# Kernel optimization log

Hardware: AMD Instinct MI355X
Metric: run time of the kernel (lower is better)

Reference implementation:

```python
import jax, jax.numpy as jnp
import numpy as np

N, D, HID, G, E2 = 2048, 256, 128, 8, 16384


def _mlp(h, w1, b1, g, be, w2, b2):
    # Linear -> ReLU -> BatchNorm1d (training mode, biased batch var) -> Linear
    h = jax.nn.relu(h @ w1 + b1)
    mu = h.mean(axis=0)
    var = ((h - mu) ** 2).mean(axis=0)
    h = (h - mu) / jnp.sqrt(var + 1e-5) * g + be
    return h @ w2 + b2


def setup_inputs() -> dict:
    key = jax.random.key(0)
    ks = jax.random.split(key, 12)
    x = jax.random.normal(ks[0], (N, D), jnp.float32)
    src = jax.random.randint(ks[1], (E2,), 0, N)
    dst = jax.random.randint(ks[2], (E2,), 0, N)
    src = jnp.where(src == dst, (src + 1) % N, src)  # no self loops
    edge_index = jnp.stack([jnp.concatenate([src, dst]),
                            jnp.concatenate([dst, src])])  # symmetric
    batch = jnp.sort(jax.random.randint(ks[3], (N,), 0, G))
    def lin(k, i, o):
        return 0.1 * jax.random.normal(k, (i, o), jnp.float32)
    out = dict(x=x, edge_index=edge_index, batch=batch)
    dims = [(1, HID, HID), (HID, HID, HID), (HID, HID, 1)]
    names = [("w11", "b11", "g1", "be1", "w12", "b12"),
             ("w21", "b21", "g2", "be2", "w22", "b22"),
             ("w31", "b31", "g3", "be3", "w32", "b32")]
    k = 4
    for (i, h, o), n in zip(dims, names):
        out[n[0]] = lin(ks[k], i, h)
        out[n[1]] = jnp.zeros((h,), jnp.float32)
        out[n[2]] = jnp.ones((h,), jnp.float32)
        out[n[3]] = jnp.zeros((h,), jnp.float32)
        out[n[4]] = lin(ks[k + 1], h, o)
        out[n[5]] = jnp.zeros((o,), jnp.float32)
        k += 2
    return out


def reference(x, edge_index, batch,
              w11, b11, g1, be1, w12, b12,
              w21, b21, g2, be2, w22, b22,
              w31, b31, g3, be3, w32, b32):
    n = x.shape[0]
    # dense adjacency from edge_index; L = D - A (unnormalized graph Laplacian)
    A = jnp.zeros((n, n), x.dtype).at[edge_index[0], edge_index[1]].set(1.0)
    deg = A.sum(axis=1)
    # entropy term: V = x*(Lx) - x*(Ax) + A(x*x), Lx = deg*x - Ax
    Ax = A @ x
    V = x * (deg[:, None] * x - Ax) - x * Ax + A @ (x * x)
    V = jnp.linalg.norm(V, axis=1)  # [n]
    # per-graph softmax over the batch segments
    mx = jax.ops.segment_max(V, batch, num_segments=G)
    ex = jnp.exp(V - mx[batch])
    P = ex / jax.ops.segment_sum(ex, batch, num_segments=G)[batch]
    P = jnp.where(P == 0.0, 1.0, P)
    ent = -P * jnp.log(P)  # [n]

    # GINConv (eps=0): mlp(x + sum_{j in N(i)} x_j) = mlp(x + A @ x)
    def gin(h, w1, b1, g, be, w2, b2):
        return _mlp(h + A @ h, w1, b1, g, be, w2, b2)

    h = gin(ent[:, None], w11, b11, g1, be1, w12, b12)
    h = gin(h, w21, b21, g2, be2, w22, b22)
    h = gin(h, w31, b31, g3, be3, w32, b32)
    p = jax.nn.sigmoid(h[:, 0])  # [n] node probabilities

    gamma = ent.sum()
    loss = gamma - jnp.vdot(ent, p) + jnp.vdot(p, A @ p)

    # greedy conditional expectation (sequential MIS-style selection)
    order = jnp.argsort(-p)

    def step(carry, idx):
        dummy, sel, rej = carry
        nb = A[idx] > 0.0  # neighbor mask [n]
        deg0 = ~jnp.any(nb)
        sel = sel.at[idx].set(sel[idx] | deg0)  # isolated node -> selected
        eligible = (~rej[idx]) & (~sel[idx])
        s = jnp.where(nb, 0.0, dummy).at[idx].set(1.0)
        li = gamma - jnp.vdot(ent, s) + jnp.vdot(s, A @ s)
        accept = eligible & (li <= loss)
        sel = sel.at[idx].set(sel[idx] | accept)
        rej = rej | (nb & accept)
        dummy = jnp.where(accept, s, dummy)
        return (dummy, sel, rej), None

    init = (p, jnp.zeros(n, dtype=bool), jnp.zeros(n, dtype=bool))
    (dummy, sel, rej), _ = jax.lax.scan(step, init, order)

    # graph reconstruction (masked instead of compacted, for static shapes)
    mask = sel.astype(x.dtype)
    x_pooled = x * mask[:, None]
    A2 = A @ A
    A3 = A2 @ A
    eye = jnp.eye(n, dtype=x.dtype)
    adj_pooled = (1.0 - eye) * jnp.clip(A2 + A3, 0.0, 1.0) * (mask[:, None] * mask[None, :])
    batch_pooled = jnp.where(sel, batch, -1)
    return x_pooled, adj_pooled, sel, batch_pooled, loss
```

## Files before the change

### kernel.cpp

```cpp
#include <hip/hip_runtime.h>
#include <math.h>

#define NN 2048
#define DIMF 256
#define HIDN 128
#define NG 8
#define NEDGES 32768
#define W32 32
#define TRI_CAP 131072
#define TRI_LDS 4864

typedef unsigned long long u64;
typedef unsigned char u8;
typedef unsigned short u16;

__global__ void k_init(u64* __restrict__ rowbits, int* __restrict__ segstart) {
  int i = blockIdx.x * blockDim.x + threadIdx.x;
  for (int k = i; k < NN * W32; k += gridDim.x * blockDim.x) rowbits[k] = 0ull;
  if (i <= NG) segstart[i] = NN;
}

__global__ void k_edges(const int* __restrict__ ei, u64* __restrict__ rowbits) {
  int e = blockIdx.x * blockDim.x + threadIdx.x;
  if (e >= NEDGES) return;
  int u = ei[e], v = ei[NEDGES + e];
  atomicOr(&rowbits[((size_t)u << 5) + (v >> 6)], 1ull << (v & 63));
}

__global__ void k_deg(const u64* __restrict__ rowbits, int* __restrict__ deg,
                      const int* __restrict__ batch, int* __restrict__ segstart) {
  int i = blockIdx.x * blockDim.x + threadIdx.x;
  if (i >= NN) return;
  int c = 0;
  for (int w = 0; w < W32; ++w) c += __popcll(rowbits[(i << 5) + w]);
  deg[i] = c;
  if (i == 0 || batch[i] != batch[i - 1]) segstart[batch[i]] = i;
}

__global__ void k_scan2048(const int* __restrict__ in, int* __restrict__ out) {
  __shared__ int part[256];
  int t = threadIdx.x;
  int v[8]; int s = 0;
  for (int k = 0; k < 8; ++k) { v[k] = in[t * 8 + k]; s += v[k]; }
  part[t] = s;
  __syncthreads();
  for (int off = 1; off < 256; off <<= 1) {
    int y = (t >= off) ? part[t - off] : 0;
    __syncthreads();
    part[t] += y;
    __syncthreads();
  }
  int run = part[t] - s;
  for (int k = 0; k < 8; ++k) { out[t * 8 + k] = run; run += v[k]; }
  if (t == 255) out[NN] = part[255];
}

__global__ void k_extract(const u64* __restrict__ rowbits, const int* __restrict__ rp,
                          int* __restrict__ col, int* __restrict__ cnt) {
  int i = blockIdx.x * blockDim.x + threadIdx.x;
  if (i >= NN) return;
  const u64* ri = rowbits + ((size_t)i << 5);
  int o = rp[i];
  for (int w = 0; w < W32; ++w) {
    u64 b = ri[w];
    while (b) { col[o++] = (w << 6) + __builtin_ctzll(b); b &= b - 1; }
  }
  int c = 0;
  for (int e = rp[i]; e < o; ++e) {
    const u64* ra = rowbits + ((size_t)col[e] << 5);
    for (int w = 0; w < W32; ++w) c += __popcll(ra[w] & ri[w]);
  }
  cnt[i] = c;
}

__global__ void k_trifill(const u64* __restrict__ rowbits, const int* __restrict__ rp,
                          const int* __restrict__ col, const int* __restrict__ tp,
                          int2* __restrict__ tri) {
  int i = blockIdx.x * blockDim.x + threadIdx.x;
  if (i >= NN) return;
  const u64* ri = rowbits + ((size_t)i << 5);
  int o = tp[i];
  for (int e = rp[i]; e < rp[i + 1]; ++e) {
    int a = col[e];
    const u64* ra = rowbits + ((size_t)a << 5);
    for (int w = 0; w < W32; ++w) {
      u64 b = ra[w] & ri[w];
      while (b) {
        int j = (w << 6) + __builtin_ctzll(b);
        if (o < TRI_CAP) tri[o] = make_int2(a, j);
        ++o;
        b &= b - 1;
      }
    }
  }
}

__global__ void k_V(const float* __restrict__ x, const int* __restrict__ rp,
                    const int* __restrict__ col, float* __restrict__ V) {
  int i = blockIdx.x; int t = threadIdx.x;
  float xi = x[i * DIMF + t];
  float s1 = 0.f, s2 = 0.f;
  int r0 = rp[i], r1 = rp[i + 1];
  for (int e = r0; e < r1; ++e) {
    float xj = x[col[e] * DIMF + t];
    s1 += xj; s2 += xj * xj;
  }
  float dg = (float)(r1 - r0);
  float val = dg * xi * xi - 2.f * xi * s1 + s2;
  __shared__ double red[DIMF];
  red[t] = (double)val * (double)val;
  __syncthreads();
  for (int off = DIMF / 2; off > 0; off >>= 1) { if (t < off) red[t] += red[t + off]; __syncthreads(); }
  if (t == 0) V[i] = (float)sqrt(red[0]);
}

__global__ void k_soft(const float* __restrict__ V, const int* __restrict__ segstart,
                       float* __restrict__ ent, double* __restrict__ seggamma) {
  int g = blockIdx.x; int t = threadIdx.x;
  int s = segstart[g];
  int e = NN;
  for (int gg = g + 1; gg <= NG; ++gg) { int v = segstart[gg]; if (v < e) e = v; }
  if (s >= e) { if (t == 0) seggamma[g] = 0.0; return; }
  __shared__ float fm[256];
  __shared__ double dd[256];
  float m = -3.0e38f;
  for (int i = s + t; i < e; i += 256) m = fmaxf(m, V[i]);
  fm[t] = m; __syncthreads();
  for (int off = 128; off > 0; off >>= 1) { if (t < off) fm[t] = fmaxf(fm[t], fm[t + off]); __syncthreads(); }
  float mx = fm[0];
  __syncthreads();
  double sum = 0.0;
  for (int i = s + t; i < e; i += 256) sum += exp((double)V[i] - (double)mx);
  dd[t] = sum; __syncthreads();
  for (int off = 128; off > 0; off >>= 1) { if (t < off) dd[t] += dd[t + off]; __syncthreads(); }
  double tot = dd[0];
  __syncthreads();
  double gs = 0.0;
  for (int i = s + t; i < e; i += 256) {
    double P = exp((double)V[i] - (double)mx) / tot;
    float ev = (P > 0.0) ? (float)(-P * log(P)) : 0.f;
    ent[i] = ev;
    gs += (double)ev;
  }
  dd[t] = gs; __syncthreads();
  for (int off = 128; off > 0; off >>= 1) { if (t < off) dd[t] += dd[t + off]; __syncthreads(); }
  if (t == 0) seggamma[g] = dd[0];
}

__global__ void k_agg1(const float* __restrict__ ent, const int* __restrict__ rp,
                       const int* __restrict__ col, float* __restrict__ agg) {
  int i = blockIdx.x * blockDim.x + threadIdx.x;
  if (i >= NN) return;
  float a = ent[i];
  for (int e = rp[i]; e < rp[i + 1]; ++e) a += ent[col[e]];
  agg[i] = a;
}

__global__ void k_lin1(const float* __restrict__ agg, const float* __restrict__ w,
                       const float* __restrict__ b, float* __restrict__ t) {
  int idx = blockIdx.x * blockDim.x + threadIdx.x;
  if (idx >= NN * HIDN) return;
  int i = idx >> 7, k = idx & 127;
  float v = agg[i] * w[k] + b[k];
  t[idx] = v > 0.f ? v : 0.f;
}

__global__ void k_bn(const float* __restrict__ t, const float* __restrict__ g,
                     const float* __restrict__ be, float* __restrict__ scale,
                     float* __restrict__ shift) {
  int k = blockIdx.x; int tid = threadIdx.x;
  __shared__ double red[256];
  double s = 0.0;
  for (int i = tid; i < NN; i += 256) s += (double)t[i * HIDN + k];
  red[tid] = s; __syncthreads();
  for (int off = 128; off > 0; off >>= 1) { if (tid < off) red[tid] += red[tid + off]; __syncthreads(); }
  double mu = red[0] / NN;
  __syncthreads();
  double v = 0.0;
  for (int i = tid; i < NN; i += 256) { double dv = (double)t[i * HIDN + k] - mu; v += dv * dv; }
  red[tid] = v; __syncthreads();
  for (int off = 128; off > 0; off >>= 1) { if (tid < off) red[tid] += red[tid + off]; __syncthreads(); }
  if (tid == 0) {
    float var = (float)(red[0] / NN);
    float sc = g[k] / sqrtf(var + 1e-5f);
    scale[k] = sc;
    shift[k] = be[k] - (float)mu * sc;
  }
}

template<int PRE, int RELU>
__global__ void k_mm(const float* __restrict__ in, const float* __restrict__ Wm,
                     const float* __restrict__ bias, const float* __restrict__ scale,
                     const float* __restrict__ shift, float* __restrict__ out) {
  __shared__ float ti[8][HIDN];
  int r0 = blockIdx.x * 8; int t = threadIdx.x;
  for (int r = 0; r < 8; ++r) {
    float v = in[(r0 + r) * HIDN + t];
    if (PRE) v = v * scale[t] + shift[t];
    ti[r][t] = v;
  }
  __syncthreads();
  float acc[8];
  #pragma unroll
  for (int r = 0; r < 8; ++r) acc[r] = 0.f;
  for (int k = 0; k < HIDN; ++k) {
    float w = Wm[k * HIDN + t];
    #pragma unroll
    for (int r = 0; r < 8; ++r) acc[r] += ti[r][k] * w;
  }
  for (int r = 0; r < 8; ++r) {
    float v = acc[r] + bias[t];
    if (RELU) v = fmaxf(v, 0.f);
    out[(r0 + r) * HIDN + t] = v;
  }
}

__global__ void k_agg128(const float* __restrict__ h, const int* __restrict__ rp,
                         const int* __restrict__ col, float* __restrict__ agg) {
  int i = blockIdx.x; int t = threadIdx.x;
  float a = h[i * HIDN + t];
  for (int e = rp[i]; e < rp[i + 1]; ++e) a += h[col[e] * HIDN + t];
  agg[i * HIDN + t] = a;
}

__global__ void k_lin3(const float* __restrict__ tn, const float* __restrict__ scale,
                       const float* __restrict__ shift, const float* __restrict__ w32,
                       const float* __restrict__ b32, float* __restrict__ p) {
  int i = blockIdx.x; int t = threadIdx.x;
  float v = (tn[i * HIDN + t] * scale[t] + shift[t]) * w32[t];
  __shared__ float red[HIDN];
  red[t] = v; __syncthreads();
  for (int off = 64; off > 0; off >>= 1) { if (t < off) red[t] += red[t + off]; __syncthreads(); }
  if (t == 0) {
    float h3 = red[0] + b32[0];
    p[i] = 1.f / (1.f + expf(-h3));
  }
}

__global__ void k_q0(const float* __restrict__ p, const float* __restrict__ ent,
                     const int* __restrict__ rp, const int* __restrict__ col,
                     float* __restrict__ q0, float* __restrict__ e0) {
  int i = blockIdx.x * blockDim.x + threadIdx.x;
  if (i >= NN) return;
  float s = 0.f, es = 0.f;
  for (int e = rp[i]; e < rp[i + 1]; ++e) {
    int j = col[e];
    float pj = p[j];
    s += pj; es += ent[j] * pj;
  }
  q0[i] = s; e0[i] = es;
}

__global__ void k_loss(const float* __restrict__ ent, const float* __restrict__ p,
                       const float* __restrict__ q0, const double* __restrict__ seggamma,
                       double* __restrict__ scal) {
  __shared__ double ra[256], rb[256];
  int t = threadIdx.x;
  double a = 0.0, b = 0.0;
  for (int i = t; i < NN; i += 256) { a += (double)ent[i] * (double)p[i]; b += (double)p[i] * (double)q0[i]; }
  ra[t] = a; rb[t] = b; __syncthreads();
  for (int off = 128; off > 0; off >>= 1) {
    if (t < off) { ra[t] += ra[t + off]; rb[t] += rb[t + off]; }
    __syncthreads();
  }
  if (t == 0) {
    double gamma = 0.0;
    for (int g = 0; g < NG; ++g) gamma += seggamma[g];
    scal[0] = gamma; scal[1] = ra[0]; scal[2] = rb[0];
    scal[3] = gamma - ra[0] + rb[0];
  }
}

__global__ void k_sort(const float* __restrict__ p, int* __restrict__ order) {
  __shared__ u64 s[NN];
  int t = threadIdx.x;
  for (int k = t; k < NN; k += 1024) {
    unsigned b = __float_as_uint(p[k]);
    unsigned ss = (b & 0x80000000u) ? ~b : (b | 0x80000000u);
    s[k] = ((u64)(~ss) << 32) | (unsigned)k;
  }
  __syncthreads();
  for (int k = 2; k <= NN; k <<= 1) {
    for (int j = k >> 1; j > 0; j >>= 1) {
      for (int i = t; i < NN; i += 1024) {
        int ixj = i ^ j;
        if (ixj > i) {
          bool up = ((i & k) == 0);
          u64 a = s[i], b = s[ixj];
          if ((a > b) == up) { s[i] = b; s[ixj] = a; }
        }
      }
      __syncthreads();
    }
  }
  order[t] = (int)(s[t] & 0xFFFFFFFFull);
  order[t + 1024] = (int)(s[t + 1024] & 0xFFFFFFFFull);
}

#define DPP2(ctrl)                                                                        \
  a += __int_as_float(__builtin_amdgcn_update_dpp(0, __float_as_int(a), ctrl, 0xf, 0xf, true)); \
  b += __int_as_float(__builtin_amdgcn_update_dpp(0, __float_as_int(b), ctrl, 0xf, 0xf, true));

__device__ __forceinline__ void red2(float& a, float& b) {
  DPP2(0x111)
  DPP2(0x112)
  DPP2(0x114)
  DPP2(0x118)
  DPP2(0x142)
  DPP2(0x143)
  a = __int_as_float(__builtin_amdgcn_readlane(__float_as_int(a), 63));
  b = __int_as_float(__builtin_amdgcn_readlane(__float_as_int(b), 63));
}

__global__ void __launch_bounds__(1024, 1) k_greedy(
    const int* __restrict__ rp, const int* __restrict__ col,
    const int* __restrict__ tp, const int2* __restrict__ tri,
    const int* __restrict__ order, const float* __restrict__ p,
    const float* __restrict__ ent, const float* __restrict__ q0,
    const float* __restrict__ e0, const double* __restrict__ scal,
    u8* __restrict__ selb_g) {
  __shared__ float2 dq[NN];
  __shared__ float2 ee[NN];
  __shared__ u16 colL[NEDGES];
  __shared__ u16 ordl[NN];
  __shared__ uint2 rtP[NN + 1];
  __shared__ ushort2 triL[TRI_LDS];
  __shared__ unsigned decidedL[64], selL[64];
  __shared__ unsigned maskL[2];
  __shared__ float4 svA[2][16];
  int t = threadIdx.x;
  int w = t >> 6, lane = t & 63;

  for (int i = t; i < NN; i += 1024) {
    dq[i] = make_float2(p[i], q0[i]);
    ee[i] = make_float2(ent[i], e0[i]);
    ordl[i] = (u16)order[i];
    int tv0 = tp[i]; if (tv0 > 65535) tv0 = 65535;
    int tv1 = tp[i + 1]; if (tv1 > 65535) tv1 = 65535;
    rtP[i] = make_uint2((unsigned)rp[i] | ((unsigned)tv0 << 16),
                        (unsigned)rp[i + 1] | ((unsigned)tv1 << 16));
  }
  for (int i = t; i < NEDGES; i += 1024) colL[i] = (u16)col[i];
  for (int i = t; i < TRI_LDS; i += 1024) {
    int2 ab = tri[i];
    triL[i] = make_ushort2((u16)(ab.x & 2047), (u16)(ab.y & 2047));
  }
  if (t < 64) { decidedL[t] = 0u; selL[t] = 0u; }
  if (t < 2) maskL[t] = 0u;
  double gamma = scal[0], loss = scal[3];
  double ed = scal[1], dAd = scal[2];
  __syncthreads();
  for (int i = t; i < NN; i += 1024) {
    if (((rtP[i].y & 0xffffu) - (rtP[i].x & 0xffffu)) == 0u) {
      atomicOr(&decidedL[i >> 5], 1u << (i & 31));
      atomicOr(&selL[i >> 5], 1u << (i & 31));
    }
  }
  __syncthreads();

  int pos = 0, rc = 0;
  while (pos < NN) {
    int b = rc & 1; ++rc;
    int step = pos + w;
    if (step < NN) {
      int idx = ordl[step];
      if (!((decidedL[idx >> 5] >> (idx & 31)) & 1u)) {
        uint2 rt = rtP[idx];
        int r0 = rt.x & 0xffff, r1 = rt.y & 0xffff;
        int t0 = rt.x >> 16, t1 = rt.y >> 16;
        float2 dqi = dq[idx];
        float2 eei = ee[idx];
        float s2 = 0.f, st = 0.f;
        for (int e = r0 + lane; e < r1; e += 64) {
          float2 v = dq[colL[e]];
          s2 -= v.y * v.x;
        }
        if (t1 <= TRI_LDS) {
          for (int e = t0 + lane; e < t1; e += 64) {
            ushort2 ab = triL[e];
            st += dq[ab.x].x * dq[ab.y].x;
          }
        } else {
          int g0 = tp[idx], g1 = tp[idx + 1];
          if (g0 > TRI_CAP) g0 = TRI_CAP;
          if (g1 > TRI_CAP) g1 = TRI_CAP;
          for (int e = g0 + lane; e < g1; e += 64) {
            int2 ab = tri[e];
            st += dq[ab.x].x * dq[ab.y].x;
          }
        }
        red2(s2, st);
        float d0 = 1.f - dqi.x;
        float S1 = -eei.y + eei.x * d0;
        float S2 = s2 + dqi.y * d0;
        float sn = -dqi.y;
        double cross = 2.0 * (double)d0 * (double)sn + (double)st;
        double li = gamma - (ed + (double)S1) + (dAd + 2.0 * (double)S2 + cross);
        if (li <= loss && lane == 0) {
          svA[b][w] = make_float4(S1, S2, d0, st);
          atomicOr(&maskL[b], 1u << w);
        }
      }
    }
    __syncthreads();
    unsigned mask = maskL[b];
    if (mask == 0u) { pos += 16; continue; }
    int k = __builtin_ctz(mask);
    int idx = ordl[pos + k];
    float4 A = svA[b][k];
    float2 dqi = dq[idx];
    uint2 rt = rtP[idx];
    int r0 = rt.x & 0xffff, r1 = rt.y & 0xffff;
    {
      double cross = 2.0 * (double)A.z * (double)(-dqi.y) + (double)A.w;
      ed += (double)A.x;
      dAd += 2.0 * (double)A.y + cross;
    }
    __syncthreads();
    if (t == 0) maskL[b] = 0u;
    for (int e = r0 + w; e < r1; e += 16) {
      int a = colL[e];
      float da = -dq[a].x;
      if (da != 0.f) {
        float ea = ee[a].x;
        uint2 art = rtP[a];
        int b0 = art.x & 0xffff, b1 = art.y & 0xffff;
        for (int eb = b0 + lane; eb < b1; eb += 64) {
          int bb = colL[eb];
          atomicAdd(&dq[bb].y, da);
          atomicAdd(&ee[bb].y, ea * da);
        }
      }
    }
    {
      float ei = ee[idx].x;
      for (int e = r0 + t; e < r1; e += 1024) {
        int bb = colL[e];
        atomicAdd(&dq[bb].y, A.z);
        atomicAdd(&ee[bb].y, ei * A.z);
      }
    }
    __syncthreads();
    if (t == 0) {
      dq[idx].x = 1.f;
      atomicOr(&decidedL[idx >> 5], 1u << (idx & 31));
      atomicOr(&selL[idx >> 5], 1u << (idx & 31));
    }
    for (int e = r0 + t; e < r1; e += 1024) {
      int j = colL[e];
      dq[j].x = 0.f;
      atomicOr(&decidedL[j >> 5], 1u << (j & 31));
    }
    __syncthreads();
    pos += k + 1;
  }
  for (int i = t; i < NN; i += 1024)
    selb_g[i] = (u8)((selL[i >> 5] >> (i & 31)) & 1u);
}

__global__ void k_reach(const u64* __restrict__ src, const int* __restrict__ rp,
                        const int* __restrict__ col, u64* __restrict__ dst) {
  int node = blockIdx.x * 2 + (threadIdx.x >> 5);
  int w = threadIdx.x & 31;
  u64 acc = 0;
  for (int e = rp[node]; e < rp[node + 1]; ++e) acc |= src[((size_t)col[e] << 5) + w];
  dst[((size_t)node << 5) + w] = acc;
}

__global__ void k_out(const u64* __restrict__ row2, const u64* __restrict__ row3,
                      const u8* __restrict__ selb, const float* __restrict__ x,
                      const int* __restrict__ batch, const double* __restrict__ scal,
                      float* __restrict__ o_x, float* __restrict__ o_adj,
                      float* __restrict__ o_sel, float* __restrict__ o_bat,
                      float* __restrict__ o_loss) {
  int idx = blockIdx.x * blockDim.x + threadIdx.x;
  {
    int i = idx >> 11, j = idx & 2047;
    int wo = (i << 5) + (j >> 6);
    u64 b = (row2[wo] | row3[wo]) >> (j & 63);
    o_adj[idx] = ((b & 1ull) && i != j && selb[i] && selb[j]) ? 1.f : 0.f;
  }
  if (idx < NN * DIMF) {
    int i = idx >> 8;
    o_x[idx] = selb[i] ? x[idx] : 0.f;
  }
  if (idx < NN) {
    o_sel[idx] = selb[idx] ? 1.f : 0.f;
    o_bat[idx] = selb[idx] ? (float)batch[idx] : -1.f;
  }
  if (idx == 0) o_loss[0] = (float)scal[3];
}

extern "C" void kernel_launch(void* const* d_in, const int* in_sizes, int n_in,
                              void* d_out, int out_size, void* d_ws, size_t ws_size,
                              hipStream_t stream) {
  const float* x    = (const float*)d_in[0];
  const int*   ei   = (const int*)d_in[1];
  const int*   batch= (const int*)d_in[2];
  const float* w11  = (const float*)d_in[3];
  const float* b11  = (const float*)d_in[4];
  const float* g1   = (const float*)d_in[5];
  const float* be1  = (const float*)d_in[6];
  const float* w12  = (const float*)d_in[7];
  const float* b12  = (const float*)d_in[8];
  const float* w21  = (const float*)d_in[9];
  const float* b21  = (const float*)d_in[10];
  const float* g2   = (const float*)d_in[11];
  const float* be2  = (const float*)d_in[12];
  const float* w22  = (const float*)d_in[13];
  const float* b22  = (const float*)d_in[14];
  const float* w31  = (const float*)d_in[15];
  const float* b31  = (const float*)d_in[16];
  const float* g3   = (const float*)d_in[17];
  const float* be3  = (const float*)d_in[18];
  const float* w32  = (const float*)d_in[19];
  const float* b32  = (const float*)d_in[20];

  char* wsb = (char*)d_ws;
  size_t cur = 0;
  auto alloc = [&](size_t bytes) -> void* {
    void* pp = wsb + cur;
    cur += (bytes + 255) & ~(size_t)255;
    return pp;
  };
  u64*    rowbits = (u64*)alloc((size_t)NN * W32 * 8);
  u64*    row2    = (u64*)alloc((size_t)NN * W32 * 8);
  u64*    row3    = (u64*)alloc((size_t)NN * W32 * 8);
  double* seggam  = (double*)alloc(NG * 8);
  double* scal    = (double*)alloc(4 * 8);
  int*    deg     = (int*)alloc(NN * 4);
  int*    rowptr  = (int*)alloc((NN + 1) * 4);
  int*    colx    = (int*)alloc(65536 * 4);
  int*    tricnt  = (int*)alloc(NN * 4);
  int*    triptr  = (int*)alloc((NN + 1) * 4);
  int2*   tri     = (int2*)alloc((size_t)TRI_CAP * 8);
  int*    segst   = (int*)alloc((NG + 1) * 4);
  int*    order   = (int*)alloc(NN * 4);
  float*  ent     = (float*)alloc(NN * 4);
  float*  V       = (float*)alloc(NN * 4);
  float*  p       = (float*)alloc(NN * 4);
  float*  q0      = (float*)alloc(NN * 4);
  float*  e0      = (float*)alloc(NN * 4);
  float*  agg1    = (float*)alloc(NN * 4);
  float*  scale   = (float*)alloc(HIDN * 4);
  float*  shift   = (float*)alloc(HIDN * 4);
  float*  tA      = (float*)alloc((size_t)NN * HIDN * 4);
  float*  tB      = (float*)alloc((size_t)NN * HIDN * 4);
  float*  tC      = (float*)alloc((size_t)NN * HIDN * 4);
  u8*     selb    = (u8*)alloc(NN);

  float* out    = (float*)d_out;
  float* o_x    = out;
  float* o_adj  = out + 524288;
  float* o_sel  = out + 4718592;
  float* o_bat  = out + 4720640;
  float* o_loss = out + 4722688;

  k_init<<<64, 256, 0, stream>>>(rowbits, segst);
  k_edges<<<128, 256, 0, stream>>>(ei, rowbits);
  k_deg<<<8, 256, 0, stream>>>(rowbits, deg, batch, segst);
  k_scan2048<<<1, 256, 0, stream>>>(deg, rowptr);
  k_extract<<<8, 256, 0, stream>>>(rowbits, rowptr, colx, tricnt);
  k_scan2048<<<1, 256, 0, stream>>>(tricnt, triptr);
  k_trifill<<<8, 256, 0, stream>>>(rowbits, rowptr, colx, triptr, tri);
  k_V<<<NN, 256, 0, stream>>>(x, rowptr, colx, V);
  k_soft<<<NG, 256, 0, stream>>>(V, segst, ent, seggam);

  k_agg1<<<8, 256, 0, stream>>>(ent, rowptr, colx, agg1);
  k_lin1<<<1024, 256, 0, stream>>>(agg1, w11, b11, tA);
  k_bn<<<HIDN, 256, 0, stream>>>(tA, g1, be1, scale, shift);
  k_mm<1, 0><<<NN / 8, HIDN, 0, stream>>>(tA, w12, b12, scale, shift, tB);
  k_agg128<<<NN, HIDN, 0, stream>>>(tB, rowptr, colx, tC);
  k_mm<0, 1><<<NN / 8, HIDN, 0, stream>>>(tC, w21, b21, scale, shift, tA);
  k_bn<<<HIDN, 256, 0, stream>>>(tA, g2, be2, scale, shift);
  k_mm<1, 0><<<NN / 8, HIDN, 0, stream>>>(tA, w22, b22, scale, shift, tB);
  k_agg128<<<NN, HIDN, 0, stream>>>(tB, rowptr, colx, tC);
  k_mm<0, 1><<<NN / 8, HIDN, 0, stream>>>(tC, w31, b31, scale, shift, tA);
  k_bn<<<HIDN, 256, 0, stream>>>(tA, g3, be3, scale, shift);
  k_lin3<<<NN, HIDN, 0, stream>>>(tA, scale, shift, w32, b32, p);

  k_q0<<<8, 256, 0, stream>>>(p, ent, rowptr, colx, q0, e0);
  k_loss<<<1, 256, 0, stream>>>(ent, p, q0, seggam, scal);
  k_sort<<<1, 1024, 0, stream>>>(p, order);
  k_greedy<<<1, 1024, 0, stream>>>(rowptr, colx, triptr, tri, order, p, ent, q0, e0, scal, selb);

  k_reach<<<NN / 2, 64, 0, stream>>>(rowbits, rowptr, colx, row2);
  k_reach<<<NN / 2, 64, 0, stream>>>(row2, rowptr, colx, row3);
  k_out<<<NN * NN / 256, 256, 0, stream>>>(row2, row3, selb, x, batch, scal,
                                           o_x, o_adj, o_sel, o_bat, o_loss);

  (void)in_sizes; (void)n_in; (void)out_size; (void)ws_size;
}
```

Measured before the change: 1.132 ms.

## Fuse q0/loss/sort into greedy kernel and compact undecided candidates per round

Moves the neighbor-sum (q0/e0), loss reduction and bitonic sort into the single-block greedy kernel, removing three serial launches and their global round trips. Each round now ballots which upcoming nodes are still undecided and gives the 16 wavefronts only undecided candidates, so rounds are not spent on already-rejected nodes. Cross terms are precomputed and stored per wave. The cost is extra per-round ballot, barrier and popcount work, plus sort and prep work now running inside one block.

New measurement: 1.945 ms. 71.8% more time.

```diff
diff --git a/kernel.cpp b/kernel.cpp
--- a/kernel.cpp
+++ b/kernel.cpp
@@ -237,66 +237,6 @@
   }
 }
 
-__global__ void k_q0(const float* __restrict__ p, const float* __restrict__ ent,
-                     const int* __restrict__ rp, const int* __restrict__ col,
-                     float* __restrict__ q0, float* __restrict__ e0) {
-  int i = blockIdx.x * blockDim.x + threadIdx.x;
-  if (i >= NN) return;
-  float s = 0.f, es = 0.f;
-  for (int e = rp[i]; e < rp[i + 1]; ++e) {
-    int j = col[e];
-    float pj = p[j];
-    s += pj; es += ent[j] * pj;
-  }
-  q0[i] = s; e0[i] = es;
-}
-
-__global__ void k_loss(const float* __restrict__ ent, const float* __restrict__ p,
-                       const float* __restrict__ q0, const double* __restrict__ seggamma,
-                       double* __restrict__ scal) {
-  __shared__ double ra[256], rb[256];
-  int t = threadIdx.x;
-  double a = 0.0, b = 0.0;
-  for (int i = t; i < NN; i += 256) { a += (double)ent[i] * (double)p[i]; b += (double)p[i] * (double)q0[i]; }
-  ra[t] = a; rb[t] = b; __syncthreads();
-  for (int off = 128; off > 0; off >>= 1) {
-    if (t < off) { ra[t] += ra[t + off]; rb[t] += rb[t + off]; }
-    __syncthreads();
-  }
-  if (t == 0) {
-    double gamma = 0.0;
-    for (int g = 0; g < NG; ++g) gamma += seggamma[g];
-    scal[0] = gamma; scal[1] = ra[0]; scal[2] = rb[0];
-    scal[3] = gamma - ra[0] + rb[0];
-  }
-}
-
-__global__ void k_sort(const float* __restrict__ p, int* __restrict__ order) {
-  __shared__ u64 s[NN];
-  int t = threadIdx.x;
-  for (int k = t; k < NN; k += 1024) {
-    unsigned b = __float_as_uint(p[k]);
-    unsigned ss = (b & 0x80000000u) ? ~b : (b | 0x80000000u);
-    s[k] = ((u64)(~ss) << 32) | (unsigned)k;
-  }
-  __syncthreads();
-  for (int k = 2; k <= NN; k <<= 1) {
-    for (int j = k >> 1; j > 0; j >>= 1) {
-      for (int i = t; i < NN; i += 1024) {
-        int ixj = i ^ j;
-        if (ixj > i) {
-          bool up = ((i & k) == 0);
-          u64 a = s[i], b = s[ixj];
-          if ((a > b) == up) { s[i] = b; s[ixj] = a; }
-        }
-      }
-      __syncthreads();
-    }
-  }
-  order[t] = (int)(s[t] & 0xFFFFFFFFull);
-  order[t + 1024] = (int)(s[t + 1024] & 0xFFFFFFFFull);
-}
-
 #define DPP2(ctrl)                                                                        \
   a += __int_as_float(__builtin_amdgcn_update_dpp(0, __float_as_int(a), ctrl, 0xf, 0xf, true)); \
   b += __int_as_float(__builtin_amdgcn_update_dpp(0, __float_as_int(b), ctrl, 0xf, 0xf, true));
@@ -312,33 +252,53 @@
   b = __int_as_float(__builtin_amdgcn_readlane(__float_as_int(b), 63));
 }
 
+__device__ __forceinline__ int nthpos(const u64* B, int slot, int pos) {
+  int cnt = 0, res = -1;
+  #pragma unroll
+  for (int i = 0; i < 16; ++i) {
+    int c = __popcll(B[i]);
+    if (res < 0 && cnt + c > slot) {
+      u64 bb = B[i];
+      int r = slot - cnt;
+      for (int k = 0; k < r; ++k) bb &= bb - 1;
+      res = pos + (i << 6) + (int)__builtin_ctzll(bb);
+    }
+    cnt += c;
+  }
+  return res;
+}
+
 __global__ void __launch_bounds__(1024, 1) k_greedy(
     const int* __restrict__ rp, const int* __restrict__ col,
     const int* __restrict__ tp, const int2* __restrict__ tri,
-    const int* __restrict__ order, const float* __restrict__ p,
-    const float* __restrict__ ent, const float* __restrict__ q0,
-    const float* __restrict__ e0, const double* __restrict__ scal,
+    const float* __restrict__ p, const float* __restrict__ ent,
+    const double* __restrict__ seggam, double* __restrict__ scal,
     u8* __restrict__ selb_g) {
   __shared__ float2 dq[NN];
   __shared__ float2 ee[NN];
   __shared__ u16 colL[NEDGES];
   __shared__ u16 ordl[NN];
-  __shared__ uint2 rtP[NN + 1];
+  __shared__ uint2 rtP[NN];
   __shared__ ushort2 triL[TRI_LDS];
+  __shared__ u64 skey[NN];
   __shared__ unsigned decidedL[64], selL[64];
+  __shared__ u64 wbalL[16];
   __shared__ unsigned maskL[2];
-  __shared__ float4 svA[2][16];
+  __shared__ float4 svB[16];
+  __shared__ double svCr[16];
+  __shared__ double redD[36];
   int t = threadIdx.x;
   int w = t >> 6, lane = t & 63;
 
   for (int i = t; i < NN; i += 1024) {
-    dq[i] = make_float2(p[i], q0[i]);
-    ee[i] = make_float2(ent[i], e0[i]);
-    ordl[i] = (u16)order[i];
+    dq[i].x = p[i]; ee[i].x = ent[i];
     int tv0 = tp[i]; if (tv0 > 65535) tv0 = 65535;
     int tv1 = tp[i + 1]; if (tv1 > 65535) tv1 = 65535;
     rtP[i] = make_uint2((unsigned)rp[i] | ((unsigned)tv0 << 16),
                         (unsigned)rp[i + 1] | ((unsigned)tv1 << 16));
+    unsigned bb = __float_as_uint(p[i]);
+    unsigned ss = (bb & 0x80000000u) ? ~bb : (bb | 0x80000000u);
+    skey[i] = ((u64)(~ss) << 32) | (unsigned)i;
   }
   for (int i = t; i < NEDGES; i += 1024) colL[i] = (u16)col[i];
   for (int i = t; i < TRI_LDS; i += 1024) {
@@ -347,77 +307,132 @@
   }
   if (t < 64) { decidedL[t] = 0u; selL[t] = 0u; }
   if (t < 2) maskL[t] = 0u;
-  double gamma = scal[0], loss = scal[3];
-  double ed = scal[1], dAd = scal[2];
-  __syncthreads();
+  __syncthreads();
+
+  for (int k = 2; k <= NN; k <<= 1) {
+    for (int j = k >> 1; j > 0; j >>= 1) {
+      for (int i = t; i < NN; i += 1024) {
+        int ixj = i ^ j;
+        if (ixj > i) {
+          bool up = ((i & k) == 0);
+          u64 a = skey[i], b = skey[ixj];
+          if ((a > b) == up) { skey[i] = b; skey[ixj] = a; }
+        }
+      }
+      __syncthreads();
+    }
+  }
+  ordl[t] = (u16)(skey[t] & 0xffffu);
+  ordl[t + 1024] = (u16)(skey[t + 1024] & 0xffffu);
+  __syncthreads();
+
+  double la = 0.0, lb = 0.0;
   for (int i = t; i < NN; i += 1024) {
-    if (((rtP[i].y & 0xffffu) - (rtP[i].x & 0xffffu)) == 0u) {
+    int r0 = rtP[i].x & 0xffff, r1 = rtP[i].y & 0xffff;
+    float qs = 0.f, es = 0.f;
+    for (int e = r0; e < r1; ++e) {
+      int j = colL[e];
+      qs += dq[j].x;
+      es += ee[j].x * dq[j].x;
+    }
+    dq[i].y = qs; ee[i].y = es;
+    la += (double)ee[i].x * (double)dq[i].x;
+    lb += (double)dq[i].x * (double)qs;
+    if (r0 == r1) {
       atomicOr(&decidedL[i >> 5], 1u << (i & 31));
       atomicOr(&selL[i >> 5], 1u << (i & 31));
     }
   }
+  for (int off = 32; off > 0; off >>= 1) { la += __shfl_down(la, off); lb += __shfl_down(lb, off); }
+  if (lane == 0) { redD[w] = la; redD[16 + w] = lb; }
+  __syncthreads();
+  if (t == 0) {
+    double A = 0.0, Bb = 0.0, gamma = 0.0;
+    for (int i = 0; i < 16; ++i) { A += redD[i]; Bb += redD[16 + i]; }
+    for (int g = 0; g < NG; ++g) gamma += seggam[g];
+    redD[32] = gamma; redD[33] = A; redD[34] = Bb; redD[35] = gamma - A + Bb;
+    scal[0] = gamma; scal[1] = A; scal[2] = Bb; scal[3] = gamma - A + Bb;
+  }
+  __syncthreads();
+  double gamma = redD[32], loss = redD[35];
+  double ed = redD[33], dAd = redD[34];
   __syncthreads();
 
   int pos = 0, rc = 0;
   while (pos < NN) {
     int b = rc & 1; ++rc;
-    int step = pos + w;
-    if (step < NN) {
-      int idx = ordl[step];
-      if (!((decidedL[idx >> 5] >> (idx & 31)) & 1u)) {
-        uint2 rt = rtP[idx];
-        int r0 = rt.x & 0xffff, r1 = rt.y & 0xffff;
-        int t0 = rt.x >> 16, t1 = rt.y >> 16;
-        float2 dqi = dq[idx];
-        float2 eei = ee[idx];
-        float s2 = 0.f, st = 0.f;
-        for (int e = r0 + lane; e < r1; e += 64) {
-          float2 v = dq[colL[e]];
-          s2 -= v.y * v.x;
+    {
+      int P = pos + t;
+      int f = 0;
+      if (P < NN) {
+        int ix = ordl[P];
+        f = !((decidedL[ix >> 5] >> (ix & 31)) & 1u);
+      }
+      u64 bal = __ballot(f);
+      if (lane == 0) wbalL[w] = bal;
+    }
+    __syncthreads();
+    u64 B[16];
+    #pragma unroll
+    for (int i = 0; i < 16; ++i) B[i] = wbalL[i];
+    int total = 0;
+    #pragma unroll
+    for (int i = 0; i < 16; ++i) total += __popcll(B[i]);
+    int myP = nthpos(B, w, pos);
+    if (myP >= 0) {
+      int idx = ordl[myP];
+      uint2 rt = rtP[idx];
+      int r0 = rt.x & 0xffff, r1 = rt.y & 0xffff;
+      int t0 = rt.x >> 16, t1 = rt.y >> 16;
+      float2 dqi = dq[idx];
+      float2 eei = ee[idx];
+      float s2 = 0.f, st = 0.f;
+      for (int e = r0 + lane; e < r1; e += 64) {
+        float2 v = dq[colL[e]];
+        s2 -= v.y * v.x;
+      }
+      if (t1 <= TRI_LDS) {
+        for (int e = t0 + lane; e < t1; e += 64) {
+          ushort2 ab = triL[e];
+          st += dq[ab.x].x * dq[ab.y].x;
         }
-        if (t1 <= TRI_LDS) {
-          for (int e = t0 + lane; e < t1; e += 64) {
-            ushort2 ab = triL[e];
-            st += dq[ab.x].x * dq[ab.y].x;
-          }
-        } else {
-          int g0 = tp[idx], g1 = tp[idx + 1];
-          if (g0 > TRI_CAP) g0 = TRI_CAP;
-          if (g1 > TRI_CAP) g1 = TRI_CAP;
-          for (int e = g0 + lane; e < g1; e += 64) {
-            int2 ab = tri[e];
-            st += dq[ab.x].x * dq[ab.y].x;
-          }
-        }
-        red2(s2, st);
-        float d0 = 1.f - dqi.x;
-        float S1 = -eei.y + eei.x * d0;
-        float S2 = s2 + dqi.y * d0;
-        float sn = -dqi.y;
-        double cross = 2.0 * (double)d0 * (double)sn + (double)st;
-        double li = gamma - (ed + (double)S1) + (dAd + 2.0 * (double)S2 + cross);
-        if (li <= loss && lane == 0) {
-          svA[b][w] = make_float4(S1, S2, d0, st);
-          atomicOr(&maskL[b], 1u << w);
+      } else {
+        int g0 = tp[idx], g1 = tp[idx + 1];
+        if (g0 > TRI_CAP) g0 = TRI_CAP;
+        if (g1 > TRI_CAP) g1 = TRI_CAP;
+        for (int e = g0 + lane; e < g1; e += 64) {
+          int2 ab = tri[e];
+          st += dq[ab.x].x * dq[ab.y].x;
         }
       }
+      red2(s2, st);
+      float d0 = 1.f - dqi.x;
+      float S1 = -eei.y + eei.x * d0;
+      float S2 = s2 + dqi.y * d0;
+      float sn = -dqi.y;
+      double cross = 2.0 * (double)d0 * (double)sn + (double)st;
+      double li = gamma - (ed + (double)S1) + (dAd + 2.0 * (double)S2 + cross);
+      if (li <= loss && lane == 0) {
+        svB[w] = make_float4(S1, S2, d0, eei.x);
+        svCr[w] = cross;
+        atomicOr(&maskL[b], 1u << w);
+      }
     }
     __syncthreads();
     unsigned mask = maskL[b];
-    if (mask == 0u) { pos += 16; continue; }
+    if (mask == 0u) {
+      pos = (total >= 16) ? nthpos(B, 15, pos) + 1 : pos + 1024;
+      continue;
+    }
     int k = __builtin_ctz(mask);
-    int idx = ordl[pos + k];
-    float4 A = svA[b][k];
-    float2 dqi = dq[idx];
+    int Pk = nthpos(B, k, pos);
+    int idx = ordl[Pk];
+    float4 A = svB[k];
+    double aCr = svCr[k];
     uint2 rt = rtP[idx];
     int r0 = rt.x & 0xffff, r1 = rt.y & 0xffff;
-    {
-      double cross = 2.0 * (double)A.z * (double)(-dqi.y) + (double)A.w;
-      ed += (double)A.x;
-      dAd += 2.0 * (double)A.y + cross;
-    }
-    __syncthreads();
-    if (t == 0) maskL[b] = 0u;
+    ed += (double)A.x;
+    dAd += 2.0 * (double)A.y + aCr;
     for (int e = r0 + w; e < r1; e += 16) {
       int a = colL[e];
       float da = -dq[a].x;
@@ -432,19 +447,17 @@
         }
       }
     }
-    {
-      float ei = ee[idx].x;
-      for (int e = r0 + t; e < r1; e += 1024) {
-        int bb = colL[e];
-        atomicAdd(&dq[bb].y, A.z);
-        atomicAdd(&ee[bb].y, ei * A.z);
-      }
+    for (int e = r0 + t; e < r1; e += 1024) {
+      int bb = colL[e];
+      atomicAdd(&dq[bb].y, A.z);
+      atomicAdd(&ee[bb].y, A.w * A.z);
     }
     __syncthreads();
     if (t == 0) {
       dq[idx].x = 1.f;
       atomicOr(&decidedL[idx >> 5], 1u << (idx & 31));
       atomicOr(&selL[idx >> 5], 1u << (idx & 31));
+      maskL[b] = 0u;
     }
     for (int e = r0 + t; e < r1; e += 1024) {
       int j = colL[e];
@@ -452,7 +465,7 @@
       atomicOr(&decidedL[j >> 5], 1u << (j & 31));
     }
     __syncthreads();
-    pos += k + 1;
+    pos = Pk + 1;
   }
   for (int i = t; i < NN; i += 1024)
     selb_g[i] = (u8)((selL[i >> 5] >> (i & 31)) & 1u);
@@ -535,12 +548,9 @@
   int*    triptr  = (int*)alloc((NN + 1) * 4);
   int2*   tri     = (int2*)alloc((size_t)TRI_CAP * 8);
   int*    segst   = (int*)alloc((NG + 1) * 4);
-  int*    order   = (int*)alloc(NN * 4);
   float*  ent     = (float*)alloc(NN * 4);
   float*  V       = (float*)alloc(NN * 4);
   float*  p       = (float*)alloc(NN * 4);
-  float*  q0      = (float*)alloc(NN * 4);
-  float*  e0      = (float*)alloc(NN * 4);
   float*  agg1    = (float*)alloc(NN * 4);
   float*  scale   = (float*)alloc(HIDN * 4);
   float*  shift   = (float*)alloc(HIDN * 4);
@@ -579,10 +589,7 @@
   k_bn<<<HIDN, 256, 0, stream>>>(tA, g3, be3, scale, shift);
   k_lin3<<<NN, HIDN, 0, stream>>>(tA, scale, shift, w32, b32, p);
 
-  k_q0<<<8, 256, 0, stream>>>(p, ent, rowptr, colx, q0, e0);
-  k_loss<<<1, 256, 0, stream>>>(ent, p, q0, seggam, scal);
-  k_sort<<<1, 1024, 0, stream>>>(p, order);
-  k_greedy<<<1, 1024, 0, stream>>>(rowptr, colx, triptr, tri, order, p, ent, q0, e0, scal, selb);
+  k_greedy<<<1, 1024, 0, stream>>>(rowptr, colx, triptr, tri, p, ent, seggam, scal, selb);
 
   k_reach<<<NN / 2, 64, 0, stream>>>(rowbits, rowptr, colx, row2);
   k_reach<<<NN / 2, 64, 0, stream>>>(row2, rowptr, colx, row3);
```
